# Kernel optimization log

Measured on AMD Instinct MI355X. Metric: run time of the kernel, lower is better.

The kernel has to match this reference:

```python
import jax, jax.numpy as jnp
import numpy as np

EPS = 1e-8

def setup_inputs() -> dict:
    key = jax.random.key(0)
    k1, k2, k3, k4 = jax.random.split(key, 4)
    b, in_c, out_c, style_c, k, h, w = 8, 512, 512, 512, 3, 64, 64
    return {
        "input": jax.random.normal(k1, (b, in_c, h, w), dtype=jnp.float32),
        "style": jax.random.normal(k2, (b, style_c), dtype=jnp.float32),
        "w_affine": jax.random.normal(k3, (in_c, style_c), dtype=jnp.float32),  # Linear weight, init N(0,1), runtime-scaled
        "b_affine": jnp.ones((1, in_c), dtype=jnp.float32),                     # Bias init_value=1.0
        "w_conv": jax.random.normal(k4, (out_c, in_c, k, k), dtype=jnp.float32),
    }

def reference(input, style, w_affine, b_affine, w_conv):
    b, in_c, h, w = input.shape
    out_c, _, kh, kw = w_conv.shape
    # Equalized-LR runtime scales (lr_mul=1):
    affine_scale = 1.0 / (w_affine.shape[1] ** 0.5)          # he_std for Linear
    conv_scale = 1.0 / ((in_c * kh * kw) ** 0.5)             # he_std for conv weight
    # affine: Linear + Bias (bias initialized to 1.0)
    s = style @ w_affine.T * affine_scale + b_affine          # [b, in_c]
    # modulate: per-sample weight tensor [b, out_c, in_c, kh, kw]
    wgt = s[:, None, :, None, None] * (w_conv * conv_scale)[None]
    # demodulate
    demod = jax.lax.rsqrt(jnp.sum(wgt * wgt, axis=(2, 3, 4), keepdims=True) + EPS)
    wgt = wgt * demod
    # grouped conv with groups = batch (stride=1, padding=1)
    x = input.reshape(1, b * in_c, h, w)
    wgt = wgt.reshape(b * out_c, in_c, kh, kw)
    out = jax.lax.conv_general_dilated(
        x, wgt,
        window_strides=(1, 1),
        padding=[(1, 1), (1, 1)],
        dimension_numbers=("NCHW", "OIHW", "NCHW"),
        feature_group_count=b,
    )
    return out.reshape(b, out_c, h, w)
```

## Files before the change

kernel.cpp:

```cpp
#include <hip/hip_runtime.h>
#include <hip/hip_bf16.h>

#define BB 8
#define CIN 512
#define COUT 512
#define HH 64
#define WW 64

#define AFF_SCALE 0.044194173824159216f
#define CONV_SCALE 0.014731391274719736f
#define CONV_SCALE2 (1.0f/4608.0f)

typedef short s16x8 __attribute__((ext_vector_type(8)));
typedef float f32x4 __attribute__((ext_vector_type(4)));
typedef float f32x16 __attribute__((ext_vector_type(16)));

__device__ __forceinline__ unsigned short f2bf(float f) {
  __hip_bfloat16 h = __float2bfloat16(f);
  return *reinterpret_cast<unsigned short*>(&h);
}

__device__ __forceinline__ void gload_lds16(const void* g, void* l) {
  __builtin_amdgcn_global_load_lds(
      (const __attribute__((address_space(1))) unsigned int*)g,
      (__attribute__((address_space(3))) unsigned int*)l, 16, 0, 0);
}

__global__ __launch_bounds__(256) void affine_kernel(
    const float* __restrict__ style, const float* __restrict__ wa,
    const float* __restrict__ ba, float* __restrict__ smod) {
  int wid  = (blockIdx.x << 2) + (threadIdx.x >> 6);
  int lane = threadIdx.x & 63;
  int b  = wid >> 9;
  int ic = wid & 511;
  const float* s = style + b * CIN;
  const float* w = wa + (size_t)ic * CIN;
  float sum = 0.f;
#pragma unroll
  for (int k = 0; k < CIN / 64; ++k) sum += s[lane + 64 * k] * w[lane + 64 * k];
#pragma unroll
  for (int off = 32; off; off >>= 1) sum += __shfl_down(sum, off, 64);
  if (lane == 0) smod[wid] = sum * AFF_SCALE + ba[ic];
}

__global__ __launch_bounds__(256) void wsq_kernel(
    const float* __restrict__ wc, float* __restrict__ wsq) {
  int i = blockIdx.x * 256 + threadIdx.x;
  const float* p = wc + (size_t)i * 9;
  float s = 0.f;
#pragma unroll
  for (int k = 0; k < 9; ++k) { float v = p[k]; s += v * v; }
  wsq[i] = s;
}

__global__ __launch_bounds__(256) void demod_kernel(
    const float* __restrict__ smod, const float* __restrict__ wsq,
    float* __restrict__ demod) {
  int wid  = (blockIdx.x << 2) + (threadIdx.x >> 6);
  int lane = threadIdx.x & 63;
  int b  = wid >> 9;
  int oc = wid & 511;
  const float* s = smod + b * CIN;
  const float* w = wsq + (size_t)oc * CIN;
  float sum = 0.f;
#pragma unroll
  for (int k = 0; k < CIN / 64; ++k) {
    float sv = s[lane + 64 * k];
    sum += sv * sv * w[lane + 64 * k];
  }
#pragma unroll
  for (int off = 32; off; off >>= 1) sum += __shfl_down(sum, off, 64);
  if (lane == 0) demod[wid] = rsqrtf(sum * CONV_SCALE2 + 1e-8f) * CONV_SCALE;
}

__global__ __launch_bounds__(256) void premod_kernel(
    const float* __restrict__ xin, const float* __restrict__ smod,
    ushort* __restrict__ xt) {
  int n = blockIdx.x * 256 + threadIdx.x;
  int kg = n & 3;
  int x  = (n >> 2) & 63;
  int y  = (n >> 8) & 63;
  int g  = (n >> 14) & 15;
  int b  = n >> 18;
  int ic0 = g * 32 + kg * 8;
  const float* sp = smod + b * CIN + ic0;
  const float* xp = xin + (((size_t)b * CIN + ic0) * HH + y) * WW + x;
  s16x8 o;
#pragma unroll
  for (int j = 0; j < 8; ++j) {
    float v = xp[(size_t)j * HH * WW] * sp[j];
    o[j] = (short)f2bf(v);
  }
  *(s16x8*)(xt + (size_t)n * 8) = o;
}

__global__ __launch_bounds__(256) void wpack_kernel(
    const float* __restrict__ wc, ushort* __restrict__ wfrag) {
  int n = blockIdx.x * 256 + threadIdx.x;
  int l    = n & 63;
  int ks   = (n >> 6) & 1;
  int mf   = (n >> 7) & 15;
  int widx = n >> 11;
  int g = widx / 9, tap = widx % 9;
  int kh = tap / 3, kw = tap - kh * 3;
  int oc  = mf * 32 + (l & 31);
  int ic0 = g * 32 + ks * 16 + 8 * (l >> 5);
  s16x8 o;
#pragma unroll
  for (int j = 0; j < 8; ++j) {
    float v = wc[((size_t)oc * CIN + ic0 + j) * 9 + kh * 3 + kw];
    o[j] = (short)f2bf(v);
  }
  *(s16x8*)(wfrag + (size_t)n * 8) = o;
}

#define XS_ROW 4224
#define XS_BUF (6 * XS_ROW)

__global__ __launch_bounds__(256, 2) void conv_mfma(
    const ushort* __restrict__ xt,
    const ushort* __restrict__ wfrag,
    const float* __restrict__ demod,
    float* __restrict__ out) {
  __shared__ char lds[2 * XS_BUF];

  int tid = threadIdx.x;
  int l = tid & 63, w = tid >> 6;
  int bid = blockIdx.x;
  int ocb = bid & 3;
  int b   = (bid >> 2) & 7;
  int yt  = bid >> 5;
  int y0  = yt * 4;

  f32x16 acc[4][2];
#pragma unroll
  for (int i = 0; i < 4; ++i)
#pragma unroll
    for (int j = 0; j < 2; ++j)
#pragma unroll
      for (int e = 0; e < 16; ++e) acc[i][j][e] = 0.f;

  if (tid < 96) {
    int buf = tid & 1, side = (tid >> 1) & 1, kgz = (tid >> 2) & 3, r = tid >> 4;
    int chunk = side ? (260 + kgz) : kgz;
    *(int4*)(lds + buf * XS_BUF + r * XS_ROW + chunk * 16) = int4{0, 0, 0, 0};
  }
  if (y0 == 0) {
    for (int i = tid; i < 512; i += 256) {
      int buf = i & 1, chunk = 4 + (i >> 1);
      *(int4*)(lds + buf * XS_BUF + chunk * 16) = int4{0, 0, 0, 0};
    }
  }
  if (y0 == 60) {
    for (int i = tid; i < 512; i += 256) {
      int buf = i & 1, chunk = 4 + (i >> 1);
      *(int4*)(lds + buf * XS_BUF + 5 * XS_ROW + chunk * 16) = int4{0, 0, 0, 0};
    }
  }

  int boffs[2][3][2];
  {
    int lm = l & 31, kh2 = l >> 5;
#pragma unroll
    for (int fn = 0; fn < 2; ++fn)
#pragma unroll
      for (int dxi = 0; dxi < 3; ++dxi)
#pragma unroll
        for (int ks = 0; ks < 2; ++ks) {
          int col = fn * 32 + lm + dxi;
          int kg  = kh2 + 2 * ks;
          boffs[fn][dxi][ks] = (col * 4 + (kg ^ ((col >> 1) & 3))) * 16;
        }
  }

  int col_s = 1 + w * 16 + (l >> 2);
  int srcoff = (col_s - 1) * 64 + ((l & 3) ^ ((col_s >> 1) & 3)) * 16;
  int lds_woff = 64 + w * 1024;

  const char* xtb = (const char*)xt;
  const char* wl = (const char*)wfrag + (size_t)ocb * 8192 + (size_t)l * 16;

  s16x8 wH[3][4];
#pragma unroll
  for (int q = 0; q < 4; ++q) wH[0][q] = *(const s16x8*)(wl + q * 2048);
#pragma unroll
  for (int q = 0; q < 4; ++q) wH[1][q] = *(const s16x8*)(wl + q * 2048 + 1024);

  {
    size_t gbase = (size_t)(b * 16) * 262144;
#pragma unroll
    for (int r = 0; r < 6; ++r) {
      int gy = y0 - 1 + r;
      if (gy >= 0 && gy < HH)
        gload_lds16(xtb + gbase + (size_t)gy * 4096 + srcoff,
                    lds + r * XS_ROW + lds_woff);
    }
  }
  __syncthreads();

  for (int g2 = 0; g2 < 8; ++g2) {
    const char* wg = wl + (size_t)g2 * 589824;
#pragma unroll
    for (int gg = 0; gg < 2; ++gg) {
      char* xs_r = lds + gg * XS_BUF;
      char* xs_w = lds + (gg ^ 1) * XS_BUF;
#pragma unroll
      for (int tap = 0; tap < 9; ++tap) {
        const int X0 = 2 * (gg * 9 + tap);

        if (tap == 6 && (gg == 0 || g2 < 7)) {
          __builtin_amdgcn_sched_barrier(0);
          size_t gbase = (size_t)(b * 16 + g2 * 2 + gg + 1) * 262144;
#pragma unroll
          for (int r = 0; r < 6; ++r) {
            int gy = y0 - 1 + r;
            if (gy >= 0 && gy < HH)
              gload_lds16(xtb + gbase + (size_t)gy * 4096 + srcoff,
                          xs_w + r * XS_ROW + lds_woff);
          }
          __builtin_amdgcn_sched_barrier(0);
        }

        const int dy = tap / 3 - 1, dxi = tap % 3;
        const int rb = w + 1 + dy;
        s16x8 bfr[2][2];
#pragma unroll
        for (int fn = 0; fn < 2; ++fn)
#pragma unroll
          for (int ks = 0; ks < 2; ++ks)
            bfr[fn][ks] = *(const s16x8*)(xs_r + rb * XS_ROW + boffs[fn][dxi][ks]);

        {
          const int u = X0 % 3, v = (X0 + 2) % 3;
          const char* wp = wg + (size_t)((X0 + 2) >> 1) * 32768 + ((X0 + 2) & 1) * 1024;
#pragma unroll
          for (int q = 0; q < 4; ++q) wH[v][q] = *(const s16x8*)(wp + q * 2048);
          __builtin_amdgcn_s_setprio(1);
#pragma unroll
          for (int q = 0; q < 4; ++q)
#pragma unroll
            for (int fn = 0; fn < 2; ++fn)
              acc[q][fn] = __builtin_amdgcn_mfma_f32_32x32x16_bf16(wH[u][q], bfr[fn][0], acc[q][fn], 0, 0, 0);
          __builtin_amdgcn_s_setprio(0);
        }
        {
          const int u = (X0 + 1) % 3, v = (X0 + 3) % 3;
          const char* wp = wg + (size_t)((X0 + 3) >> 1) * 32768 + ((X0 + 3) & 1) * 1024;
#pragma unroll
          for (int q = 0; q < 4; ++q) wH[v][q] = *(const s16x8*)(wp + q * 2048);
          __builtin_amdgcn_s_setprio(1);
#pragma unroll
          for (int q = 0; q < 4; ++q)
#pragma unroll
            for (int fn = 0; fn < 2; ++fn)
              acc[q][fn] = __builtin_amdgcn_mfma_f32_32x32x16_bf16(wH[u][q], bfr[fn][1], acc[q][fn], 0, 0, 0);
          __builtin_amdgcn_s_setprio(0);
        }

        if (tap == 8 && (gg == 0 || g2 < 7)) {
          __builtin_amdgcn_sched_barrier(0);
          asm volatile("s_waitcnt vmcnt(8)" ::: "memory");
          __builtin_amdgcn_sched_barrier(0);
          __builtin_amdgcn_s_barrier();
          __builtin_amdgcn_sched_barrier(0);
        }
      }
    }
  }

  int gy = y0 + w;
  int colbase = l & 31;
  int rowadd = 4 * (l >> 5);
#pragma unroll
  for (int q = 0; q < 4; ++q) {
#pragma unroll
    for (int reg = 0; reg < 16; ++reg) {
      int row = (reg & 3) + 8 * (reg >> 2) + rowadd;
      int oc = ocb * 128 + q * 32 + row;
      float dm = demod[b * COUT + oc];
      size_t obase = ((size_t)(b * COUT + oc)) * 4096 + gy * 64;
      out[obase + colbase]      = acc[q][0][reg] * dm;
      out[obase + 32 + colbase] = acc[q][1][reg] * dm;
    }
  }
}

extern "C" void kernel_launch(void* const* d_in, const int* in_sizes, int n_in,
                              void* d_out, int out_size, void* d_ws, size_t ws_size,
                              hipStream_t stream) {
  const float* input = (const float*)d_in[0];
  const float* style = (const float*)d_in[1];
  const float* wa    = (const float*)d_in[2];
  const float* ba    = (const float*)d_in[3];
  const float* wconv = (const float*)d_in[4];
  float* out = (float*)d_out;

  float* smod  = (float*)d_ws;
  float* demod = smod + BB * CIN;
  float* wsq   = demod + BB * COUT;
  ushort* wfrag = (ushort*)(wsq + (size_t)COUT * CIN);
  ushort* xt    = wfrag + (size_t)16 * 9 * 32 * 64 * 8;

  affine_kernel<<<BB * CIN / 4, 256, 0, stream>>>(style, wa, ba, smod);
  wsq_kernel<<<COUT * CIN / 256, 256, 0, stream>>>(wconv, wsq);
  demod_kernel<<<BB * COUT / 4, 256, 0, stream>>>(smod, wsq, demod);
  wpack_kernel<<<16 * 9 * 32 * 64 / 256, 256, 0, stream>>>(wconv, wfrag);
  premod_kernel<<<BB * 16 * 64 * 64 * 4 / 256, 256, 0, stream>>>(input, smod, xt);
  conv_mfma<<<BB * 4 * 16, 256, 0, stream>>>(xt, wfrag, demod, out);
}
```

Measured before the change: 162.2 us.

## Retile conv waves as 2x2 over out-channels and rows, prefetch LDS B fragments

Each wave now computes 64 output channels by two image rows (two OC fragments by four pixel fragments) instead of 128 channels by one row. This halves the per-wave global weight-fragment loads and doubles the per-wave LDS activation reads. The first-k-half B fragments are double-buffered and loaded one tap ahead, and the vmcnt wait is adjusted to match the smaller number of weight loads in flight. Register pressure shifts from weight fragments to activation fragments.

New measurement: 156.2 us. 1.04x faster.

```diff
diff --git a/kernel.cpp b/kernel.cpp
--- a/kernel.cpp
+++ b/kernel.cpp
@@ -12,7 +12,6 @@
 #define CONV_SCALE2 (1.0f/4608.0f)
 
 typedef short s16x8 __attribute__((ext_vector_type(8)));
-typedef float f32x4 __attribute__((ext_vector_type(4)));
 typedef float f32x16 __attribute__((ext_vector_type(16)));
 
 __device__ __forceinline__ unsigned short f2bf(float f) {
@@ -126,17 +125,18 @@
 
   int tid = threadIdx.x;
   int l = tid & 63, w = tid >> 6;
+  int wm = w >> 1, wr = w & 1;
   int bid = blockIdx.x;
   int ocb = bid & 3;
   int b   = (bid >> 2) & 7;
   int yt  = bid >> 5;
   int y0  = yt * 4;
 
-  f32x16 acc[4][2];
-#pragma unroll
-  for (int i = 0; i < 4; ++i)
-#pragma unroll
-    for (int j = 0; j < 2; ++j)
+  f32x16 acc[2][4];
+#pragma unroll
+  for (int i = 0; i < 2; ++i)
+#pragma unroll
+    for (int j = 0; j < 4; ++j)
 #pragma unroll
       for (int e = 0; e < 16; ++e) acc[i][j][e] = 0.f;
 
@@ -162,14 +162,14 @@
   {
     int lm = l & 31, kh2 = l >> 5;
 #pragma unroll
-    for (int fn = 0; fn < 2; ++fn)
+    for (int ph = 0; ph < 2; ++ph)
 #pragma unroll
       for (int dxi = 0; dxi < 3; ++dxi)
 #pragma unroll
         for (int ks = 0; ks < 2; ++ks) {
-          int col = fn * 32 + lm + dxi;
+          int col = ph * 32 + lm + dxi;
           int kg  = kh2 + 2 * ks;
-          boffs[fn][dxi][ks] = (col * 4 + (kg ^ ((col >> 1) & 3))) * 16;
+          boffs[ph][dxi][ks] = (col * 4 + (kg ^ ((col >> 1) & 3))) * 16;
         }
   }
 
@@ -178,13 +178,13 @@
   int lds_woff = 64 + w * 1024;
 
   const char* xtb = (const char*)xt;
-  const char* wl = (const char*)wfrag + (size_t)ocb * 8192 + (size_t)l * 16;
-
-  s16x8 wH[3][4];
-#pragma unroll
-  for (int q = 0; q < 4; ++q) wH[0][q] = *(const s16x8*)(wl + q * 2048);
-#pragma unroll
-  for (int q = 0; q < 4; ++q) wH[1][q] = *(const s16x8*)(wl + q * 2048 + 1024);
+  const char* wl = (const char*)wfrag + (size_t)(ocb * 4 + wm * 2) * 2048 + (size_t)l * 16;
+
+  s16x8 wH[3][2];
+#pragma unroll
+  for (int q = 0; q < 2; ++q) wH[0][q] = *(const s16x8*)(wl + q * 2048);
+#pragma unroll
+  for (int q = 0; q < 2; ++q) wH[1][q] = *(const s16x8*)(wl + q * 2048 + 1024);
 
   {
     size_t gbase = (size_t)(b * 16) * 262144;
@@ -198,6 +198,9 @@
   }
   __syncthreads();
 
+  s16x8 bfr0[2][4];
+  s16x8 bfr1[4];
+
   for (int g2 = 0; g2 < 8; ++g2) {
     const char* wg = wl + (size_t)g2 * 589824;
 #pragma unroll
@@ -207,6 +210,17 @@
 #pragma unroll
       for (int tap = 0; tap < 9; ++tap) {
         const int X0 = 2 * (gg * 9 + tap);
+        const int dy = tap / 3 - 1, dxi = tap % 3;
+        const int rb = wr * 2 + 1 + dy;
+
+        if (tap == 0) {
+#pragma unroll
+          for (int dr = 0; dr < 2; ++dr)
+#pragma unroll
+            for (int ph = 0; ph < 2; ++ph)
+              bfr0[0][dr * 2 + ph] =
+                  *(const s16x8*)(xs_r + (rb + dr) * XS_ROW + boffs[ph][dxi][0]);
+        }
 
         if (tap == 6 && (gg == 0 || g2 < 7)) {
           __builtin_amdgcn_sched_barrier(0);
@@ -221,45 +235,57 @@
           __builtin_amdgcn_sched_barrier(0);
         }
 
-        const int dy = tap / 3 - 1, dxi = tap % 3;
-        const int rb = w + 1 + dy;
-        s16x8 bfr[2][2];
-#pragma unroll
-        for (int fn = 0; fn < 2; ++fn)
-#pragma unroll
-          for (int ks = 0; ks < 2; ++ks)
-            bfr[fn][ks] = *(const s16x8*)(xs_r + rb * XS_ROW + boffs[fn][dxi][ks]);
+#pragma unroll
+        for (int dr = 0; dr < 2; ++dr)
+#pragma unroll
+          for (int ph = 0; ph < 2; ++ph)
+            bfr1[dr * 2 + ph] =
+                *(const s16x8*)(xs_r + (rb + dr) * XS_ROW + boffs[ph][dxi][1]);
 
         {
-          const int u = X0 % 3, v = (X0 + 2) % 3;
           const char* wp = wg + (size_t)((X0 + 2) >> 1) * 32768 + ((X0 + 2) & 1) * 1024;
 #pragma unroll
-          for (int q = 0; q < 4; ++q) wH[v][q] = *(const s16x8*)(wp + q * 2048);
+          for (int q = 0; q < 2; ++q)
+            wH[(X0 + 2) % 3][q] = *(const s16x8*)(wp + q * 2048);
           __builtin_amdgcn_s_setprio(1);
 #pragma unroll
-          for (int q = 0; q < 4; ++q)
-#pragma unroll
-            for (int fn = 0; fn < 2; ++fn)
-              acc[q][fn] = __builtin_amdgcn_mfma_f32_32x32x16_bf16(wH[u][q], bfr[fn][0], acc[q][fn], 0, 0, 0);
+          for (int q = 0; q < 2; ++q)
+#pragma unroll
+            for (int n = 0; n < 4; ++n)
+              acc[q][n] = __builtin_amdgcn_mfma_f32_32x32x16_bf16(
+                  wH[X0 % 3][q], bfr0[tap & 1][n], acc[q][n], 0, 0, 0);
           __builtin_amdgcn_s_setprio(0);
         }
+
+        if (tap < 8) {
+          const int dyn = (tap + 1) / 3 - 1, dxn = (tap + 1) % 3;
+          const int rbn = wr * 2 + 1 + dyn;
+#pragma unroll
+          for (int dr = 0; dr < 2; ++dr)
+#pragma unroll
+            for (int ph = 0; ph < 2; ++ph)
+              bfr0[(tap + 1) & 1][dr * 2 + ph] =
+                  *(const s16x8*)(xs_r + (rbn + dr) * XS_ROW + boffs[ph][dxn][0]);
+        }
+
         {
-          const int u = (X0 + 1) % 3, v = (X0 + 3) % 3;
           const char* wp = wg + (size_t)((X0 + 3) >> 1) * 32768 + ((X0 + 3) & 1) * 1024;
 #pragma unroll
-          for (int q = 0; q < 4; ++q) wH[v][q] = *(const s16x8*)(wp + q * 2048);
+          for (int q = 0; q < 2; ++q)
+            wH[(X0 + 3) % 3][q] = *(const s16x8*)(wp + q * 2048);
           __builtin_amdgcn_s_setprio(1);
 #pragma unroll
-          for (int q = 0; q < 4; ++q)
-#pragma unroll
-            for (int fn = 0; fn < 2; ++fn)
-              acc[q][fn] = __builtin_amdgcn_mfma_f32_32x32x16_bf16(wH[u][q], bfr[fn][1], acc[q][fn], 0, 0, 0);
+          for (int q = 0; q < 2; ++q)
+#pragma unroll
+            for (int n = 0; n < 4; ++n)
+              acc[q][n] = __builtin_amdgcn_mfma_f32_32x32x16_bf16(
+                  wH[(X0 + 1) % 3][q], bfr1[n], acc[q][n], 0, 0, 0);
           __builtin_amdgcn_s_setprio(0);
         }
 
         if (tap == 8 && (gg == 0 || g2 < 7)) {
           __builtin_amdgcn_sched_barrier(0);
-          asm volatile("s_waitcnt vmcnt(8)" ::: "memory");
+          asm volatile("s_waitcnt vmcnt(4)" ::: "memory");
           __builtin_amdgcn_sched_barrier(0);
           __builtin_amdgcn_s_barrier();
           __builtin_amdgcn_sched_barrier(0);
@@ -268,19 +294,22 @@
     }
   }
 
-  int gy = y0 + w;
+  int gy_base = y0 + wr * 2;
   int colbase = l & 31;
   int rowadd = 4 * (l >> 5);
 #pragma unroll
-  for (int q = 0; q < 4; ++q) {
+  for (int q = 0; q < 2; ++q) {
 #pragma unroll
     for (int reg = 0; reg < 16; ++reg) {
       int row = (reg & 3) + 8 * (reg >> 2) + rowadd;
-      int oc = ocb * 128 + q * 32 + row;
+      int oc = ocb * 128 + (wm * 2 + q) * 32 + row;
       float dm = demod[b * COUT + oc];
-      size_t obase = ((size_t)(b * COUT + oc)) * 4096 + gy * 64;
-      out[obase + colbase]      = acc[q][0][reg] * dm;
-      out[obase + 32 + colbase] = acc[q][1][reg] * dm;
+#pragma unroll
+      for (int n = 0; n < 4; ++n) {
+        int gy = gy_base + (n >> 1);
+        int px = (n & 1) * 32 + colbase;
+        out[((size_t)(b * COUT + oc)) * 4096 + gy * 64 + px] = acc[q][n][reg] * dm;
+      }
     }
   }
 }
```
